# Kernel optimization log

Hardware: AMD Instinct MI355X
Metric: run time of the kernel (lower is better)

## Reference

```python
import jax, jax.numpy as jnp
import numpy as np

SPHERE_RADIUS = 1.0
DISTANCE_ERROR = 0.002
BIG = 1e10  # sentinel for 'no intersection'


def setup_inputs() -> dict:
    key = jax.random.key(0)
    k1, k2 = jax.random.split(key)
    x = jax.random.normal(k1, (1, 1048576, 7), dtype=jnp.float32)
    z = jax.random.normal(k2, (1, 384), dtype=jnp.float32)
    return {"x": x, "z": z}


def reference(x, z):
    # x: [B, N, 7] = origin(3), time(1), direction(3)
    # z: [B, 6*S]  = per-sphere center(3), velocity(3)
    B, N, _ = x.shape
    origin = x[..., 0:3]                      # [B, N, 3]
    t_ray = x[..., 3:4]                       # [B, N, 1] ray time
    direction = x[..., 4:7]                   # [B, N, 3]
    d = direction / (jnp.linalg.norm(direction, axis=-1, keepdims=True) + 1e-12)

    spheres = z.reshape(B, -1, 6)             # [B, S, 6]
    sph_c = spheres[..., 0:3]                 # [B, S, 3]
    sph_v = spheres[..., 3:6]                 # [B, S, 3]

    # play sphere forward to ray time: center(t) = c + v * t  -> [B, N, S, 3]
    center_t = sph_c[:, None, :, :] + sph_v[:, None, :, :] * t_ray[..., None]

    oc = center_t - origin[:, :, None, :]     # [B, N, S, 3]
    b = jnp.einsum('bnd,bnsd->bns', d, oc)    # projection of oc on ray dir
    c = jnp.einsum('bnsd,bnsd->bns', oc, oc) - SPHERE_RADIUS * SPHERE_RADIUS
    disc = b * b - c                          # [B, N, S]

    sq = jnp.sqrt(jnp.where(disc > 0, disc, 1.0))  # safe sqrt
    t0 = b - sq
    t1 = b + sq
    t_hit = jnp.where(t0 > 0, t0, t1)         # nearest non-negative root
    valid = (disc >= 0) & (t1 > 0)
    dist = jnp.where(valid, t_hit, BIG)       # [B, N, S]

    closest = jnp.min(dist, axis=-1)          # min-distance reduction over spheres
    mu = closest.reshape(1, N, 1)
    sigma = jnp.full((1, N, 1), DISTANCE_ERROR, dtype=x.dtype)
    return mu, sigma
```

## Files before the change

kernel.cpp:

```cpp
#include <hip/hip_runtime.h>


typedef float v2f __attribute__((ext_vector_type(2)));

constexpr float BIGF = 1e10f;

__global__ __launch_bounds__(256, 8) void ray_sphere_kernel(
    const float* __restrict__ x, const float* __restrict__ z,
    float* __restrict__ out, int N)
{
    int tid = blockIdx.x * 256 + threadIdx.x;
    long n0 = (long)tid * 2;
    if (n0 >= N) return;

    const float2* xr = (const float2*)(x + n0 * 7);
    float2 w0 = xr[0], w1 = xr[1], w2 = xr[2], w3 = xr[3],
           w4 = xr[4], w5 = xr[5], w6 = xr[6];

    v2f ox = {w0.x, w3.y}, oy = {w0.y, w4.x}, oz = {w1.x, w4.y};
    v2f t  = {w1.y, w5.x};
    v2f dx = {w2.x, w5.y}, dy = {w2.y, w6.x}, dz = {w3.x, w6.y};

    {
        v2f n2 = __builtin_elementwise_fma(dx, dx,
                 __builtin_elementwise_fma(dy, dy, dz * dz));
        v2f inv;
        inv[0] = __builtin_amdgcn_rcpf(__builtin_amdgcn_sqrtf(n2[0]) + 1e-12f);
        inv[1] = __builtin_amdgcn_rcpf(__builtin_amdgcn_sqrtf(n2[1]) + 1e-12f);
        dx *= inv; dy *= inv; dz *= inv;
    }

    v2f closest = {BIGF, BIGF};

    int s0 = (blockIdx.x & 7) << 3;

    #pragma unroll
    for (int j = 0; j < 8; ++j) {
        const float* zg = z + ((s0 + (j << 3)) & 63) * 6;
        #pragma unroll
        for (int k = 0; k < 8; ++k) {
            const float* zs = zg + k * 6;
            float cx = zs[0], cy = zs[1], cz = zs[2];
            float vx = zs[3], vy = zs[4], vz = zs[5];

            v2f ocx = __builtin_elementwise_fma((v2f){vx, vx}, t, cx - ox);
            v2f ocy = __builtin_elementwise_fma((v2f){vy, vy}, t, cy - oy);
            v2f ocz = __builtin_elementwise_fma((v2f){vz, vz}, t, cz - oz);
            v2f b = __builtin_elementwise_fma(dx, ocx,
                    __builtin_elementwise_fma(dy, ocy, dz * ocz));
            v2f csq = __builtin_elementwise_fma(ocx, ocx,
                      __builtin_elementwise_fma(ocy, ocy, ocz * ocz));
            v2f disc = __builtin_elementwise_fma(b, b, (v2f){1.0f, 1.0f} - csq);

            v2f sq;
            sq[0] = __builtin_amdgcn_sqrtf(disc[0]);
            sq[1] = __builtin_amdgcn_sqrtf(disc[1]);

            v2f t0 = b - sq;
            v2f t1 = b + sq;

            #pragma unroll
            for (int kk = 0; kk < 2; ++kk) {
                float r1 = (t1[kk] > 0.0f) ? t1[kk] : BIGF;
                float r  = (t0[kk] > 0.0f) ? t0[kk] : r1;
                closest[kk] = fminf(closest[kk], r);
            }
        }
    }

    *(float2*)(out + n0) = make_float2(closest[0], closest[1]);
    *(float2*)(out + N + n0) = make_float2(0.002f, 0.002f);
}

extern "C" void kernel_launch(void* const* d_in, const int* in_sizes, int n_in,
                              void* d_out, int out_size, void* d_ws, size_t ws_size,
                              hipStream_t stream) {
    const float* x = (const float*)d_in[0];
    const float* z = (const float*)d_in[1];
    float* out = (float*)d_out;
    int N = in_sizes[0] / 7;

    int threads = N / 2;
    int blocks = (threads + 255) / 256;
    ray_sphere_kernel<<<blocks, 256, 0, stream>>>(x, z, out, N);
}
```

Measured before the change: 34.33 us.

## Stage spheres in transposed LDS and pack sphere pairs into v2f lanes

Result: no change. 34.77 us (+1.3%).

```diff
diff --git a/kernel.cpp b/kernel.cpp
--- a/kernel.cpp
+++ b/kernel.cpp
@@ -5,70 +5,109 @@
 
 constexpr float BIGF = 1e10f;
 
-__global__ __launch_bounds__(256, 8) void ray_sphere_kernel(
+__global__ __launch_bounds__(256, 4) void ray_sphere_kernel(
     const float* __restrict__ x, const float* __restrict__ z,
     float* __restrict__ out, int N)
 {
-    int tid = blockIdx.x * 256 + threadIdx.x;
-    long n0 = (long)tid * 2;
-    if (n0 >= N) return;
+    __shared__ float zp[6][64];
+
+    int tidb = threadIdx.x;
+    int tid  = blockIdx.x * 256 + tidb;
+    long n0  = (long)tid * 2;
 
     const float2* xr = (const float2*)(x + n0 * 7);
     float2 w0 = xr[0], w1 = xr[1], w2 = xr[2], w3 = xr[3],
            w4 = xr[4], w5 = xr[5], w6 = xr[6];
 
-    v2f ox = {w0.x, w3.y}, oy = {w0.y, w4.x}, oz = {w1.x, w4.y};
-    v2f t  = {w1.y, w5.x};
-    v2f dx = {w2.x, w5.y}, dy = {w2.y, w6.x}, dz = {w3.x, w6.y};
+    {
+        int i = tidb;
+        int s = i / 6, c = i - s * 6;
+        zp[c][s] = z[i];
+        if (tidb < 128) {
+            int i2 = tidb + 256;
+            int s2 = i2 / 6, c2 = i2 - s2 * 6;
+            zp[c2][s2] = z[i2];
+        }
+    }
+    __syncthreads();
+
+    float ox0 = w0.x, oy0 = w0.y, oz0 = w1.x, tr0 = w1.y,
+          dx0 = w2.x, dy0 = w2.y, dz0 = w3.x;
+    float ox1 = w3.y, oy1 = w4.x, oz1 = w4.y, tr1 = w5.x,
+          dx1 = w5.y, dy1 = w6.x, dz1 = w6.y;
 
     {
-        v2f n2 = __builtin_elementwise_fma(dx, dx,
-                 __builtin_elementwise_fma(dy, dy, dz * dz));
-        v2f inv;
-        inv[0] = __builtin_amdgcn_rcpf(__builtin_amdgcn_sqrtf(n2[0]) + 1e-12f);
-        inv[1] = __builtin_amdgcn_rcpf(__builtin_amdgcn_sqrtf(n2[1]) + 1e-12f);
-        dx *= inv; dy *= inv; dz *= inv;
+        float n2 = fmaf(dx0, dx0, fmaf(dy0, dy0, dz0 * dz0));
+        float inv = __builtin_amdgcn_rcpf(__builtin_amdgcn_sqrtf(n2) + 1e-12f);
+        dx0 *= inv; dy0 *= inv; dz0 *= inv;
+    }
+    {
+        float n2 = fmaf(dx1, dx1, fmaf(dy1, dy1, dz1 * dz1));
+        float inv = __builtin_amdgcn_rcpf(__builtin_amdgcn_sqrtf(n2) + 1e-12f);
+        dx1 *= inv; dy1 *= inv; dz1 *= inv;
     }
 
-    v2f closest = {BIGF, BIGF};
+    v2f oxA = {ox0, ox0}, oyA = {oy0, oy0}, ozA = {oz0, oz0}, tA = {tr0, tr0};
+    v2f dxA = {dx0, dx0}, dyA = {dy0, dy0}, dzA = {dz0, dz0};
+    v2f oxB = {ox1, ox1}, oyB = {oy1, oy1}, ozB = {oz1, oz1}, tB = {tr1, tr1};
+    v2f dxB = {dx1, dx1}, dyB = {dy1, dy1}, dzB = {dz1, dz1};
 
-    int s0 = (blockIdx.x & 7) << 3;
+    float clA = BIGF, clB = BIGF;
 
-    #pragma unroll
-    for (int j = 0; j < 8; ++j) {
-        const float* zg = z + ((s0 + (j << 3)) & 63) * 6;
-        #pragma unroll
-        for (int k = 0; k < 8; ++k) {
-            const float* zs = zg + k * 6;
-            float cx = zs[0], cy = zs[1], cz = zs[2];
-            float vx = zs[3], vy = zs[4], vz = zs[5];
+    #pragma unroll 8
+    for (int j = 0; j < 32; ++j) {
+        v2f cx = *(const v2f*)&zp[0][2 * j];
+        v2f cy = *(const v2f*)&zp[1][2 * j];
+        v2f cz = *(const v2f*)&zp[2][2 * j];
+        v2f vx = *(const v2f*)&zp[3][2 * j];
+        v2f vy = *(const v2f*)&zp[4][2 * j];
+        v2f vz = *(const v2f*)&zp[5][2 * j];
 
-            v2f ocx = __builtin_elementwise_fma((v2f){vx, vx}, t, cx - ox);
-            v2f ocy = __builtin_elementwise_fma((v2f){vy, vy}, t, cy - oy);
-            v2f ocz = __builtin_elementwise_fma((v2f){vz, vz}, t, cz - oz);
-            v2f b = __builtin_elementwise_fma(dx, ocx,
-                    __builtin_elementwise_fma(dy, ocy, dz * ocz));
+        {
+            v2f ocx = __builtin_elementwise_fma(vx, tA, cx - oxA);
+            v2f ocy = __builtin_elementwise_fma(vy, tA, cy - oyA);
+            v2f ocz = __builtin_elementwise_fma(vz, tA, cz - ozA);
+            v2f b   = __builtin_elementwise_fma(dxA, ocx,
+                      __builtin_elementwise_fma(dyA, ocy, dzA * ocz));
             v2f csq = __builtin_elementwise_fma(ocx, ocx,
                       __builtin_elementwise_fma(ocy, ocy, ocz * ocz));
             v2f disc = __builtin_elementwise_fma(b, b, (v2f){1.0f, 1.0f} - csq);
-
             v2f sq;
             sq[0] = __builtin_amdgcn_sqrtf(disc[0]);
             sq[1] = __builtin_amdgcn_sqrtf(disc[1]);
-
             v2f t0 = b - sq;
             v2f t1 = b + sq;
-
             #pragma unroll
-            for (int kk = 0; kk < 2; ++kk) {
-                float r1 = (t1[kk] > 0.0f) ? t1[kk] : BIGF;
-                float r  = (t0[kk] > 0.0f) ? t0[kk] : r1;
-                closest[kk] = fminf(closest[kk], r);
+            for (int k = 0; k < 2; ++k) {
+                float r1 = (t1[k] > 0.0f) ? t1[k] : BIGF;
+                float r  = (t0[k] > 0.0f) ? t0[k] : r1;
+                clA = fminf(clA, r);
+            }
+        }
+        {
+            v2f ocx = __builtin_elementwise_fma(vx, tB, cx - oxB);
+            v2f ocy = __builtin_elementwise_fma(vy, tB, cy - oyB);
+            v2f ocz = __builtin_elementwise_fma(vz, tB, cz - ozB);
+            v2f b   = __builtin_elementwise_fma(dxB, ocx,
+                      __builtin_elementwise_fma(dyB, ocy, dzB * ocz));
+            v2f csq = __builtin_elementwise_fma(ocx, ocx,
+                      __builtin_elementwise_fma(ocy, ocy, ocz * ocz));
+            v2f disc = __builtin_elementwise_fma(b, b, (v2f){1.0f, 1.0f} - csq);
+            v2f sq;
+            sq[0] = __builtin_amdgcn_sqrtf(disc[0]);
+            sq[1] = __builtin_amdgcn_sqrtf(disc[1]);
+            v2f t0 = b - sq;
+            v2f t1 = b + sq;
+            #pragma unroll
+            for (int k = 0; k < 2; ++k) {
+                float r1 = (t1[k] > 0.0f) ? t1[k] : BIGF;
+                float r  = (t0[k] > 0.0f) ? t0[k] : r1;
+                clB = fminf(clB, r);
             }
         }
     }
 
-    *(float2*)(out + n0) = make_float2(closest[0], closest[1]);
+    *(float2*)(out + n0)     = make_float2(clA, clB);
     *(float2*)(out + N + n0) = make_float2(0.002f, 0.002f);
 }
 
```

## Stage ray inputs through padded LDS with coalesced loads

Applied to the files above, without the earlier changes.

Measured after the change: 35.56 us. 1.04x slower.

```diff
diff --git a/kernel.cpp b/kernel.cpp
--- a/kernel.cpp
+++ b/kernel.cpp
@@ -4,22 +4,35 @@
 typedef float v2f __attribute__((ext_vector_type(2)));
 
 constexpr float BIGF = 1e10f;
+constexpr int BLK = 256;
+constexpr int RPB = 512;
+constexpr int STR = 9;
 
-__global__ __launch_bounds__(256, 8) void ray_sphere_kernel(
+__global__ __launch_bounds__(BLK, 8) void ray_sphere_kernel(
     const float* __restrict__ x, const float* __restrict__ z,
     float* __restrict__ out, int N)
 {
-    int tid = blockIdx.x * 256 + threadIdx.x;
-    long n0 = (long)tid * 2;
-    if (n0 >= N) return;
+    __shared__ float lds[RPB * STR];
 
-    const float2* xr = (const float2*)(x + n0 * 7);
-    float2 w0 = xr[0], w1 = xr[1], w2 = xr[2], w3 = xr[3],
-           w4 = xr[4], w5 = xr[5], w6 = xr[6];
+    const int t = threadIdx.x;
+    const long blockRay0 = (long)blockIdx.x * RPB;
 
-    v2f ox = {w0.x, w3.y}, oy = {w0.y, w4.x}, oz = {w1.x, w4.y};
-    v2f t  = {w1.y, w5.x};
-    v2f dx = {w2.x, w5.y}, dy = {w2.y, w6.x}, dz = {w3.x, w6.y};
+    const float* xs = x + blockRay0 * 7;
+    #pragma unroll
+    for (int k = 0; k < 14; ++k) {
+        unsigned i = (unsigned)(k * BLK + t);
+        float v = xs[i];
+        unsigned r = i / 7u;
+        unsigned j = i - r * 7u;
+        lds[r * STR + j] = v;
+    }
+    __syncthreads();
+
+    const float* r0 = lds + (2 * t) * STR;
+    const float* r1 = r0 + STR;
+    v2f ox = {r0[0], r1[0]}, oy = {r0[1], r1[1]}, oz = {r0[2], r1[2]};
+    v2f tr = {r0[3], r1[3]};
+    v2f dx = {r0[4], r1[4]}, dy = {r0[5], r1[5]}, dz = {r0[6], r1[6]};
 
     {
         v2f n2 = __builtin_elementwise_fma(dx, dx,
@@ -32,43 +45,38 @@
 
     v2f closest = {BIGF, BIGF};
 
-    int s0 = (blockIdx.x & 7) << 3;
+    #pragma unroll 16
+    for (int s = 0; s < 64; ++s) {
+        const float* zs = z + s * 6;
+        float cx = zs[0], cy = zs[1], cz = zs[2];
+        float vx = zs[3], vy = zs[4], vz = zs[5];
 
-    #pragma unroll
-    for (int j = 0; j < 8; ++j) {
-        const float* zg = z + ((s0 + (j << 3)) & 63) * 6;
+        v2f ocx = __builtin_elementwise_fma((v2f){vx, vx}, tr, cx - ox);
+        v2f ocy = __builtin_elementwise_fma((v2f){vy, vy}, tr, cy - oy);
+        v2f ocz = __builtin_elementwise_fma((v2f){vz, vz}, tr, cz - oz);
+        v2f b = __builtin_elementwise_fma(dx, ocx,
+                __builtin_elementwise_fma(dy, ocy, dz * ocz));
+        v2f csq = __builtin_elementwise_fma(ocx, ocx,
+                  __builtin_elementwise_fma(ocy, ocy, ocz * ocz));
+        v2f disc = __builtin_elementwise_fma(b, b, (v2f){1.0f, 1.0f} - csq);
+
+        v2f sq;
+        sq[0] = __builtin_amdgcn_sqrtf(disc[0]);
+        sq[1] = __builtin_amdgcn_sqrtf(disc[1]);
+
+        v2f t0 = b - sq;
+        v2f t1 = b + sq;
+
         #pragma unroll
-        for (int k = 0; k < 8; ++k) {
-            const float* zs = zg + k * 6;
-            float cx = zs[0], cy = zs[1], cz = zs[2];
-            float vx = zs[3], vy = zs[4], vz = zs[5];
-
-            v2f ocx = __builtin_elementwise_fma((v2f){vx, vx}, t, cx - ox);
-            v2f ocy = __builtin_elementwise_fma((v2f){vy, vy}, t, cy - oy);
-            v2f ocz = __builtin_elementwise_fma((v2f){vz, vz}, t, cz - oz);
-            v2f b = __builtin_elementwise_fma(dx, ocx,
-                    __builtin_elementwise_fma(dy, ocy, dz * ocz));
-            v2f csq = __builtin_elementwise_fma(ocx, ocx,
-                      __builtin_elementwise_fma(ocy, ocy, ocz * ocz));
-            v2f disc = __builtin_elementwise_fma(b, b, (v2f){1.0f, 1.0f} - csq);
-
-            v2f sq;
-            sq[0] = __builtin_amdgcn_sqrtf(disc[0]);
-            sq[1] = __builtin_amdgcn_sqrtf(disc[1]);
-
-            v2f t0 = b - sq;
-            v2f t1 = b + sq;
-
-            #pragma unroll
-            for (int kk = 0; kk < 2; ++kk) {
-                float r1 = (t1[kk] > 0.0f) ? t1[kk] : BIGF;
-                float r  = (t0[kk] > 0.0f) ? t0[kk] : r1;
-                closest[kk] = fminf(closest[kk], r);
-            }
+        for (int k = 0; k < 2; ++k) {
+            float r1v = (t1[k] > 0.0f) ? t1[k] : BIGF;
+            float rr  = (t0[k] > 0.0f) ? t0[k] : r1v;
+            closest[k] = fminf(closest[k], rr);
         }
     }
 
-    *(float2*)(out + n0) = make_float2(closest[0], closest[1]);
+    long n0 = blockRay0 + 2 * t;
+    *(float2*)(out + n0)     = make_float2(closest[0], closest[1]);
     *(float2*)(out + N + n0) = make_float2(0.002f, 0.002f);
 }
 
@@ -80,7 +88,6 @@
     float* out = (float*)d_out;
     int N = in_sizes[0] / 7;
 
-    int threads = N / 2;
-    int blocks = (threads + 255) / 256;
-    ray_sphere_kernel<<<blocks, 256, 0, stream>>>(x, z, out, N);
+    int blocks = N / RPB;
+    ray_sphere_kernel<<<blocks, BLK, 0, stream>>>(x, z, out, N);
 }
```
